# Kernel optimization log

Measured on AMD Instinct MI355X. Metric: run time of the kernel, lower is better.

The kernel has to match this reference:

```python
import jax, jax.numpy as jnp
import numpy as np

B, C, H, W = 16, 256, 64, 64
E = 8           # num_experts
TOPK = 2
HID = int(C * 2.0)  # hidden_mult = 2.0 -> 512


def setup_inputs() -> dict:
    key = jax.random.key(0)
    ks = jax.random.split(key, 6)
    x = jax.random.normal(ks[0], (B, C, H, W), dtype=jnp.float32)
    Wr = jax.random.normal(ks[1], (C, E), dtype=jnp.float32) * 0.02
    br = jnp.zeros((E,), dtype=jnp.float32)
    W1 = jax.random.normal(ks[2], (E, C, HID), dtype=jnp.float32) * 0.02
    b1 = jnp.zeros((E, HID), dtype=jnp.float32)
    W2 = jax.random.normal(ks[3], (E, HID, C), dtype=jnp.float32) * 0.02
    b2 = jnp.zeros((E, C), dtype=jnp.float32)
    # nn.Parameter(torch.zeros(1)) in the original; use a small random value so
    scale = jax.random.normal(ks[4], (1,), dtype=jnp.float32) * 0.1
    return {"x": x, "Wr": Wr, "br": br, "W1": W1, "b1": b1,
            "W2": W2, "b2": b2, "scale": scale}


def reference(x, Wr, br, W1, b1, W2, b2, scale):
    b, c, h, w = x.shape
    tokens = jnp.transpose(x, (0, 2, 3, 1)).reshape(b, h * w, c)  # (B, T, C)
    logits = tokens @ Wr + br                                      # (B, T, E)
    topv, topi = jax.lax.top_k(logits, TOPK)                       # (B, T, K)
    wts = jax.nn.softmax(topv, axis=-1)                            # (B, T, K)

    out = jnp.zeros_like(tokens)
    num_experts = Wr.shape[1]
    for e in range(num_experts):
        # combine weight for expert e: sum of routing weights where selected
        we = jnp.sum(jnp.where(topi == e, wts, 0.0), axis=-1)      # (B, T)
        hdn = jax.nn.gelu(tokens @ W1[e] + b1[e], approximate=False)
        y = hdn @ W2[e] + b2[e]                                    # (B, T, C)
        out = out + y * we[..., None]

    out = jnp.transpose(out.reshape(b, h, w, c), (0, 3, 1, 2))     # (B, C, H, W)
    return x + scale[0] * out
```

## Files before the change

### kernel.cpp

```cpp
#include <hip/hip_runtime.h>
#include <hip/hip_bf16.h>
#include <math.h>

#define HW   4096
#define CCH  256
#define NE   8
#define HID  512
#define NTOK 65536
#define PADH 260

typedef short s16x8 __attribute__((ext_vector_type(8)));
typedef float f32x4 __attribute__((ext_vector_type(4)));
typedef unsigned short u16x8 __attribute__((ext_vector_type(8)));

__device__ __forceinline__ float fast_gelu(float v) {
    float v2 = v * v;
    float s  = v * fmaf(0.10294324f, v2, 2.3022079f);
    float e  = exp2f(-s);
    return v * __builtin_amdgcn_rcpf(1.0f + e);
}

__device__ __forceinline__ float bfbits2f(unsigned short h) {
    return __uint_as_float(((unsigned)h) << 16);
}

__device__ __forceinline__ short f2bf_bits(float f) {
    __hip_bfloat16 b = __float2bfloat16(f);
    return *reinterpret_cast<short*>(&b);
}

__global__ __launch_bounds__(256) void k_transpose_both(
    const float* __restrict__ W1, const float* __restrict__ W2,
    __hip_bfloat16* __restrict__ w1t, __hip_bfloat16* __restrict__ w2t,
    int* __restrict__ meta)
{
    __shared__ float t[64][65];
    if (blockIdx.x == 0 && threadIdx.x < 16) meta[threadIdx.x] = 0;
    int bb = blockIdx.x;
    const float* in; __hip_bfloat16* out; int R, CC;
    if (bb < 256) { in = W1; out = w1t; R = 256; CC = 512; }
    else          { in = W2; out = w2t; R = 512; CC = 256; bb -= 256; }
    int tilesC = CC >> 6;
    int per = (R >> 6) * tilesC;
    int e = bb / per, tt = bb % per;
    int r0 = (tt / tilesC) << 6, c0 = (tt % tilesC) << 6;
    const float* ip = in + (size_t)e * R * CC;
    __hip_bfloat16* op = out + (size_t)e * R * CC;
    int lane = threadIdx.x & 63, g = threadIdx.x >> 6;
    for (int i = 0; i < 16; i++) {
        int r = i * 4 + g;
        t[r][lane] = ip[(size_t)(r0 + r) * CC + c0 + lane];
    }
    __syncthreads();
    for (int i = 0; i < 16; i++) {
        int r = i * 4 + g;
        op[(size_t)(c0 + r) * R + r0 + lane] = __float2bfloat16(t[lane][r]);
    }
}

__global__ __launch_bounds__(256) void k_router(
    const float* __restrict__ x, const float* __restrict__ Wr, const float* __restrict__ br,
    __hip_bfloat16* __restrict__ tokens, int* __restrict__ pair, float2* __restrict__ wts,
    int* __restrict__ meta )
{
    __shared__ float xt[CCH][66];
    __shared__ float wr[CCH][NE];
    __shared__ float lg[64][NE];
    __shared__ int lc[NE];
    int tid = threadIdx.x;
    int n0 = blockIdx.x * 64;
    int b = n0 >> 12, p0 = n0 & 4095;
    const float* xb = x + (size_t)b * CCH * HW + p0;
    for (int i = tid; i < CCH * NE; i += 256) ((float*)wr)[i] = Wr[i];
    if (tid < NE) lc[tid] = 0;
    int lane = tid & 63, wv = tid >> 6;
    {
        int j2 = tid & 31, cg = tid >> 5;
        for (int i = 0; i < 32; i++) {
            int c = cg + 8 * i;
            float2 v = *(const float2*)(xb + (size_t)c * HW + 2 * j2);
            *(float2*)&xt[c][2 * j2] = v;
        }
    }
    __syncthreads();
    float a0 = br[2 * wv], a1 = br[2 * wv + 1];
    for (int c = 0; c < CCH; c++) {
        float xv = xt[c][lane];
        a0 = fmaf(xv, wr[c][2 * wv], a0);
        a1 = fmaf(xv, wr[c][2 * wv + 1], a1);
    }
    lg[lane][2 * wv] = a0;
    lg[lane][2 * wv + 1] = a1;
    __syncthreads();
    if (wv == 0) {
        float v0 = -1e30f, v1 = -1e30f; int i0 = 0, i1 = 0;
        for (int e = 0; e < NE; e++) {
            float l = lg[lane][e];
            if (l > v0)      { v1 = v0; i1 = i0; v0 = l; i0 = e; }
            else if (l > v1) { v1 = l; i1 = e; }
        }
        float e1 = expf(v1 - v0);
        float s = 1.0f + e1;
        wts[n0 + lane] = make_float2(1.0f / s, e1 / s);
        pair[n0 + lane] = i0 | (i1 << 8);
        atomicAdd(&lc[i0], 1);
        atomicAdd(&lc[i1], 1);
    }
    __syncthreads();
    if (tid < NE && lc[tid] > 0) atomicAdd(&meta[tid], lc[tid]);
    {
        int r = tid & 63, gb = tid >> 6;
        for (int i = 0; i < 8; i++) {
            int c0 = gb * 64 + i * 8;
            s16x8 v;
#pragma unroll
            for (int j = 0; j < 8; j++) v[j] = f2bf_bits(xt[c0 + j][r]);
            *(s16x8*)(tokens + (size_t)(n0 + r) * CCH + c0) = v;
        }
    }
}

__global__ __launch_bounds__(256) void k_scatter(
    const int* __restrict__ pair, const float2* __restrict__ wts,
    int* __restrict__ meta, int* __restrict__ assign_tok, float* __restrict__ assign_w,
    int2* __restrict__ tok_slots)
{
    __shared__ int lcount[NE];
    __shared__ int lbase[NE];
    __shared__ int soff[NE];
    int tid = threadIdx.x;
    int n = blockIdx.x * 256 + tid;
    if (tid < NE) lcount[tid] = 0;
    __syncthreads();
    int pr = pair[n];
    int e0 = pr & 0xff, e1 = (pr >> 8) & 0xff;
    int p0 = atomicAdd(&lcount[e0], 1);
    int p1 = atomicAdd(&lcount[e1], 1);
    __syncthreads();
    if (tid == 0) {
        int off = 0, toff = 0;
        for (int ee = 0; ee < NE; ee++) {
            soff[ee] = off;
            int c = meta[ee];
            if (blockIdx.x == 0) { meta[16 + ee] = off; meta[25 + ee] = toff; }
            off += c;
            toff += (c + 63) >> 6;
        }
        if (blockIdx.x == 0) { meta[24] = off; meta[33] = toff; meta[34] = toff; }
    }
    if (tid < NE) lbase[tid] = atomicAdd(&meta[8 + tid], lcount[tid]);
    __syncthreads();
    float2 w = wts[n];
    int s0 = soff[e0] + lbase[e0] + p0;
    int s1 = soff[e1] + lbase[e1] + p1;
    assign_tok[s0] = n; assign_w[s0] = w.x;
    assign_tok[s1] = n; assign_w[s1] = w.y;
    tok_slots[n] = make_int2(s0, s1);
}

__global__ __launch_bounds__(512, 4) void k_expert(
    const __hip_bfloat16* __restrict__ tokens,
    const __hip_bfloat16* __restrict__ w1t,
    const __hip_bfloat16* __restrict__ w2t,
    const float* __restrict__ b1, const float* __restrict__ b2,
    const int* __restrict__ meta,
    const int* __restrict__ assign_tok, const float* __restrict__ assign_w,
    __hip_bfloat16* __restrict__ ybuf)
{
    __shared__ __align__(16) __hip_bfloat16 Af[64 * 256];
    __shared__ __align__(16) __hip_bfloat16 Hs[64 * PADH];
    __shared__ float wrow[64];
    __shared__ int trow[64];

    int total = meta[34];
    int swz = (int)blockIdx.x;
    int bid = (swz & 7) * 257 + (swz >> 3);
    if (bid >= total) return;
    int e = 0;
    while (e < 7 && bid >= meta[25 + e + 1]) e++;
    int tile = bid - meta[25 + e];
    int cnt = meta[e];
    int r0 = tile << 6;
    int abase = meta[16 + e] + r0;
    int nrows = cnt - r0; if (nrows > 64) nrows = 64;

    int tid = threadIdx.x;
    if (tid < 64) {
        if (tid < nrows) { trow[tid] = assign_tok[abase + tid]; wrow[tid] = assign_w[abase + tid]; }
        else             { trow[tid] = 0; wrow[tid] = 0.0f; }
    }
    __syncthreads();

    {
        uint4* dst = (uint4*)Af;
#pragma unroll
        for (int j = 0; j < 4; j++) {
            int row = j * 16 + (tid & 15);
            int chunk = (tid >> 4) & 31;
            dst[j * 512 + tid] = ((const uint4*)(tokens + (size_t)trow[row] * CCH))[chunk];
        }
    }

    int lane = tid & 63, wv = tid >> 6;
    int quad = lane >> 4, l15 = lane & 15;

    const __hip_bfloat16* w1e = w1t + (size_t)e * HID * CCH;
    const __hip_bfloat16* w2e = w2t + (size_t)e * CCH * HID;
    const float* b1e = b1 + e * HID;
    const float* b2e = b2 + e * CCH;

    const s16x8* apb = (const s16x8*)Af + quad * 16 + l15;

    auto G1Q = [&](int h, int off) {
        return (const s16x8*)(w1e + (size_t)(h * 256 + wv * 32 + off + l15) * CCH) + quad;
    };
    auto G2Q = [&](int h, int off) {
        return (const s16x8*)(w2e + (size_t)(wv * 32 + off + l15) * HID + h * 256) + quad;
    };

    int hfirst = (swz >> 8) & 1;

    f32x4 oacc[4][2];
#pragma unroll
    for (int i = 0; i < 4; i++)
#pragma unroll
        for (int j = 0; j < 2; j++) oacc[i][j] = (f32x4){0.f, 0.f, 0.f, 0.f};

    s16x8 bf0 = G1Q(hfirst, 0)[0], bf1 = G1Q(hfirst, 16)[0];
    float ob0 = b2e[wv * 32 + l15];
    float ob1 = b2e[wv * 32 + 16 + l15];

    __syncthreads();

#pragma unroll
    for (int hh = 0; hh < 2; hh++) {
        int h = hh ^ hfirst;
        const s16x8* bq0 = G1Q(h, 0);
        const s16x8* bq1 = G1Q(h, 16);

        f32x4 hacc[4][2];
#pragma unroll
        for (int i = 0; i < 4; i++)
#pragma unroll
            for (int j = 0; j < 2; j++) hacc[i][j] = (f32x4){0.f, 0.f, 0.f, 0.f};

#pragma unroll
        for (int kk = 0; kk < 8; kk++) {
            s16x8 bn0, bn1;
            if (kk < 7) { bn0 = bq0[(kk + 1) * 4]; bn1 = bq1[(kk + 1) * 4]; }
            s16x8 af[4];
#pragma unroll
            for (int mt = 0; mt < 4; mt++) af[mt] = apb[mt * 512 + kk * 4 * 16];
            __builtin_amdgcn_s_setprio(1);
#pragma unroll
            for (int mt = 0; mt < 4; mt++) {
                hacc[mt][0] = __builtin_amdgcn_mfma_f32_16x16x32_bf16(af[mt], bf0, hacc[mt][0], 0, 0, 0);
                hacc[mt][1] = __builtin_amdgcn_mfma_f32_16x16x32_bf16(af[mt], bf1, hacc[mt][1], 0, 0, 0);
            }
            __builtin_amdgcn_s_setprio(0);
            bf0 = bn0; bf1 = bn1;
        }

        const s16x8* b2q0 = G2Q(h, 0);
        const s16x8* b2q1 = G2Q(h, 16);
        s16x8 cf0 = b2q0[0], cf1 = b2q1[0];
        float biasA = b1e[h * 256 + wv * 32 + l15];
        float biasB = b1e[h * 256 + wv * 32 + 16 + l15];
        if (hh == 0) { int h2 = h ^ 1; bf0 = G1Q(h2, 0)[0]; bf1 = G1Q(h2, 16)[0]; }

        if (hh == 1) __syncthreads();

#pragma unroll
        for (int nt = 0; nt < 2; nt++) {
            int cl = wv * 32 + nt * 16 + l15;
            float bias = nt ? biasB : biasA;
#pragma unroll
            for (int mt = 0; mt < 4; mt++)
#pragma unroll
                for (int r = 0; r < 4; r++) {
                    int row = mt * 16 + quad * 4 + r;
                    float v = hacc[mt][nt][r] + bias;
                    Hs[row * PADH + cl] = __float2bfloat16(fast_gelu(v));
                }
        }
        __syncthreads();

#pragma unroll
        for (int kk = 0; kk < 8; kk++) {
            s16x8 cn0, cn1;
            if (kk < 7) { cn0 = b2q0[(kk + 1) * 4]; cn1 = b2q1[(kk + 1) * 4]; }
            s16x8 hf[4];
#pragma unroll
            for (int mt = 0; mt < 4; mt++)
                hf[mt] = *(const s16x8*)(Hs + (mt * 16 + l15) * PADH + kk * 32 + quad * 8);
            __builtin_amdgcn_s_setprio(1);
#pragma unroll
            for (int mt = 0; mt < 4; mt++) {
                oacc[mt][0] = __builtin_amdgcn_mfma_f32_16x16x32_bf16(hf[mt], cf0, oacc[mt][0], 0, 0, 0);
                oacc[mt][1] = __builtin_amdgcn_mfma_f32_16x16x32_bf16(hf[mt], cf1, oacc[mt][1], 0, 0, 0);
            }
            __builtin_amdgcn_s_setprio(0);
            cf0 = cn0; cf1 = cn1;
        }
    }

#pragma unroll
    for (int nt = 0; nt < 2; nt++) {
        int cc = wv * 32 + nt * 16 + l15;
        float bias = nt ? ob1 : ob0;
#pragma unroll
        for (int mt = 0; mt < 4; mt++) {
#pragma unroll
            for (int r = 0; r < 4; r++) {
                int row = mt * 16 + quad * 4 + r;
                if (row < nrows) {
                    float v = (oacc[mt][nt][r] + bias) * wrow[row];
                    ybuf[(size_t)(abase + row) * CCH + cc] = __float2bfloat16(v);
                }
            }
        }
    }
}

__global__ __launch_bounds__(256) void k_combine(
    const float* __restrict__ x, const __hip_bfloat16* __restrict__ ybuf,
    const int2* __restrict__ tok_slots, const float* __restrict__ scale,
    float* __restrict__ out)
{
    __shared__ float moe[CCH][33];
    __shared__ int2 slots[32];
    int tid = threadIdx.x;
    int n0 = blockIdx.x * 32;
    if (tid < 32) slots[tid] = tok_slots[n0 + tid];
    __syncthreads();
    {
        int r = tid & 31, g0 = tid >> 5;
#pragma unroll
        for (int it = 0; it < 2; it++) {
            int g = g0 + 8 * it;
            int2 s = slots[r];
            const u16x8* px = (const u16x8*)(ybuf + (size_t)s.x * CCH + 16 * g);
            const u16x8* py = (const u16x8*)(ybuf + (size_t)s.y * CCH + 16 * g);
            u16x8 ax0 = px[0], ax1 = px[1], ay0 = py[0], ay1 = py[1];
#pragma unroll
            for (int k = 0; k < 8; k++) {
                moe[16 * g + k][r]     = bfbits2f(ax0[k]) + bfbits2f(ay0[k]);
                moe[16 * g + 8 + k][r] = bfbits2f(ax1[k]) + bfbits2f(ay1[k]);
            }
        }
    }
    __syncthreads();
    float sc = scale[0];
    int b = n0 >> 12, p0 = n0 & 4095;
    const float* xb = x + (size_t)b * CCH * HW + p0;
    float* ob = out + (size_t)b * CCH * HW + p0;
    int j = tid & 7, cbase = tid >> 3;
#pragma unroll
    for (int i = 0; i < 8; i++) {
        int c = cbase + 32 * i;
        float4 xv = *(const float4*)(xb + (size_t)c * HW + 4 * j);
        float4 o;
        o.x = xv.x + sc * moe[c][4 * j];
        o.y = xv.y + sc * moe[c][4 * j + 1];
        o.z = xv.z + sc * moe[c][4 * j + 2];
        o.w = xv.w + sc * moe[c][4 * j + 3];
        *(float4*)(ob + (size_t)c * HW + 4 * j) = o;
    }
}

extern "C" void kernel_launch(void* const* d_in, const int* in_sizes, int n_in,
                              void* d_out, int out_size, void* d_ws, size_t ws_size,
                              hipStream_t stream)
{
    const float* x     = (const float*)d_in[0];
    const float* Wr    = (const float*)d_in[1];
    const float* br    = (const float*)d_in[2];
    const float* W1    = (const float*)d_in[3];
    const float* b1    = (const float*)d_in[4];
    const float* W2    = (const float*)d_in[5];
    const float* b2    = (const float*)d_in[6];
    const float* scale = (const float*)d_in[7];
    float* out = (float*)d_out;

    char* ws = (char*)d_ws;
    __hip_bfloat16* tokens = (__hip_bfloat16*)(ws);
    __hip_bfloat16* w1t    = (__hip_bfloat16*)(ws + 33554432);
    __hip_bfloat16* w2t    = (__hip_bfloat16*)(ws + 35651584);
    __hip_bfloat16* ybuf   = (__hip_bfloat16*)(ws + 37748736);
    int*    assign_tok = (int*)   (ws + 104857600);
    float*  assign_w   = (float*) (ws + 105381888);
    int2*   tok_slots  = (int2*)  (ws + 105906176);
    int*    pair       = (int*)   (ws + 106430464);
    float2* wts        = (float2*)(ws + 106692608);
    int*    meta       = (int*)   (ws + 107216896);

    k_transpose_both<<<512, 256, 0, stream>>>(W1, W2, w1t, w2t, meta);
    k_router<<<1024, 256, 0, stream>>>(x, Wr, br, tokens, pair, wts, meta);
    k_scatter<<<256, 256, 0, stream>>>(pair, wts, meta, assign_tok, assign_w, tok_slots);
    k_expert<<<2056, 512, 0, stream>>>(tokens, w1t, w2t, b1, b2, meta,
                                       assign_tok, assign_w, ybuf);
    k_combine<<<2048, 256, 0, stream>>>(x, ybuf, tok_slots, scale, out);
}
```

Baseline: 343.5 us.

## Restructure router into 32-token blocks, store combine staging as bf16, drop h swizzle

```diff
diff --git a/kernel.cpp b/kernel.cpp
--- a/kernel.cpp
+++ b/kernel.cpp
@@ -12,6 +12,7 @@
 typedef short s16x8 __attribute__((ext_vector_type(8)));
 typedef float f32x4 __attribute__((ext_vector_type(4)));
 typedef unsigned short u16x8 __attribute__((ext_vector_type(8)));
+typedef unsigned short u16x4 __attribute__((ext_vector_type(4)));
 
 __device__ __forceinline__ float fast_gelu(float v) {
     float v2 = v * v;
@@ -27,6 +28,11 @@
 __device__ __forceinline__ short f2bf_bits(float f) {
     __hip_bfloat16 b = __float2bfloat16(f);
     return *reinterpret_cast<short*>(&b);
+}
+
+__device__ __forceinline__ unsigned short f2bf_ubits(float f) {
+    __hip_bfloat16 b = __float2bfloat16(f);
+    return *reinterpret_cast<unsigned short*>(&b);
 }
 
 __global__ __launch_bounds__(256) void k_transpose_both(
@@ -63,60 +69,72 @@
     __hip_bfloat16* __restrict__ tokens, int* __restrict__ pair, float2* __restrict__ wts,
     int* __restrict__ meta )
 {
-    __shared__ float xt[CCH][66];
-    __shared__ float wr[CCH][NE];
-    __shared__ float lg[64][NE];
+    __shared__ float xt[CCH][33];
+    __shared__ float wrp[2304];
+    __shared__ float lg[32][NE];
     __shared__ int lc[NE];
     int tid = threadIdx.x;
-    int n0 = blockIdx.x * 64;
+    int n0 = blockIdx.x * 32;
     int b = n0 >> 12, p0 = n0 & 4095;
     const float* xb = x + (size_t)b * CCH * HW + p0;
-    for (int i = tid; i < CCH * NE; i += 256) ((float*)wr)[i] = Wr[i];
+    for (int i = tid; i < CCH * NE; i += 256) wrp[i] = Wr[i];
     if (tid < NE) lc[tid] = 0;
-    int lane = tid & 63, wv = tid >> 6;
+    __syncthreads();
+    int j = tid & 31, cg = tid >> 5;
+    float pacc[8];
+#pragma unroll
+    for (int e = 0; e < 8; e++) pacc[e] = 0.f;
+    for (int i = 0; i < 32; i++) {
+        int c = cg + 8 * i;
+        float xv = xb[(size_t)c * HW + j];
+        xt[c][j] = xv;
+        const float4* wp = (const float4*)(wrp + c * 8);
+        float4 wa = wp[0], wb2 = wp[1];
+        pacc[0] = fmaf(xv, wa.x, pacc[0]);
+        pacc[1] = fmaf(xv, wa.y, pacc[1]);
+        pacc[2] = fmaf(xv, wa.z, pacc[2]);
+        pacc[3] = fmaf(xv, wa.w, pacc[3]);
+        pacc[4] = fmaf(xv, wb2.x, pacc[4]);
+        pacc[5] = fmaf(xv, wb2.y, pacc[5]);
+        pacc[6] = fmaf(xv, wb2.z, pacc[6]);
+        pacc[7] = fmaf(xv, wb2.w, pacc[7]);
+    }
+    __syncthreads();
+    float* plg = wrp;
+#pragma unroll
+    for (int e = 0; e < 8; e++) plg[(cg * 32 + j) * 9 + e] = pacc[e];
+    __syncthreads();
     {
-        int j2 = tid & 31, cg = tid >> 5;
-        for (int i = 0; i < 32; i++) {
-            int c = cg + 8 * i;
-            float2 v = *(const float2*)(xb + (size_t)c * HW + 2 * j2);
-            *(float2*)&xt[c][2 * j2] = v;
-        }
-    }
-    __syncthreads();
-    float a0 = br[2 * wv], a1 = br[2 * wv + 1];
-    for (int c = 0; c < CCH; c++) {
-        float xv = xt[c][lane];
-        a0 = fmaf(xv, wr[c][2 * wv], a0);
-        a1 = fmaf(xv, wr[c][2 * wv + 1], a1);
-    }
-    lg[lane][2 * wv] = a0;
-    lg[lane][2 * wv + 1] = a1;
-    __syncthreads();
-    if (wv == 0) {
+        int jj = tid & 31, e = tid >> 5;
+        float s = br[e];
+#pragma unroll
+        for (int g = 0; g < 8; g++) s += plg[(g * 32 + jj) * 9 + e];
+        lg[jj][e] = s;
+    }
+    __syncthreads();
+    if (tid < 32) {
         float v0 = -1e30f, v1 = -1e30f; int i0 = 0, i1 = 0;
         for (int e = 0; e < NE; e++) {
-            float l = lg[lane][e];
+            float l = lg[tid][e];
             if (l > v0)      { v1 = v0; i1 = i0; v0 = l; i0 = e; }
             else if (l > v1) { v1 = l; i1 = e; }
         }
         float e1 = expf(v1 - v0);
         float s = 1.0f + e1;
-        wts[n0 + lane] = make_float2(1.0f / s, e1 / s);
-        pair[n0 + lane] = i0 | (i1 << 8);
+        wts[n0 + tid] = make_float2(1.0f / s, e1 / s);
+        pair[n0 + tid] = i0 | (i1 << 8);
         atomicAdd(&lc[i0], 1);
         atomicAdd(&lc[i1], 1);
     }
     __syncthreads();
     if (tid < NE && lc[tid] > 0) atomicAdd(&meta[tid], lc[tid]);
-    {
-        int r = tid & 63, gb = tid >> 6;
-        for (int i = 0; i < 8; i++) {
-            int c0 = gb * 64 + i * 8;
-            s16x8 v;
-#pragma unroll
-            for (int j = 0; j < 8; j++) v[j] = f2bf_bits(xt[c0 + j][r]);
-            *(s16x8*)(tokens + (size_t)(n0 + r) * CCH + c0) = v;
-        }
+#pragma unroll
+    for (int i = 0; i < 4; i++) {
+        int c0 = (cg + 8 * i) * 8;
+        s16x8 v;
+#pragma unroll
+        for (int k = 0; k < 8; k++) v[k] = f2bf_bits(xt[c0 + k][j]);
+        *(s16x8*)(tokens + (size_t)(n0 + j) * CCH + c0) = v;
     }
 }
 
@@ -218,23 +236,20 @@
         return (const s16x8*)(w2e + (size_t)(wv * 32 + off + l15) * HID + h * 256) + quad;
     };
 
-    int hfirst = (swz >> 8) & 1;
-
     f32x4 oacc[4][2];
 #pragma unroll
     for (int i = 0; i < 4; i++)
 #pragma unroll
         for (int j = 0; j < 2; j++) oacc[i][j] = (f32x4){0.f, 0.f, 0.f, 0.f};
 
-    s16x8 bf0 = G1Q(hfirst, 0)[0], bf1 = G1Q(hfirst, 16)[0];
+    s16x8 bf0 = G1Q(0, 0)[0], bf1 = G1Q(0, 16)[0];
     float ob0 = b2e[wv * 32 + l15];
     float ob1 = b2e[wv * 32 + 16 + l15];
 
     __syncthreads();
 
 #pragma unroll
-    for (int hh = 0; hh < 2; hh++) {
-        int h = hh ^ hfirst;
+    for (int h = 0; h < 2; h++) {
         const s16x8* bq0 = G1Q(h, 0);
         const s16x8* bq1 = G1Q(h, 16);
 
@@ -266,9 +281,9 @@
         s16x8 cf0 = b2q0[0], cf1 = b2q1[0];
         float biasA = b1e[h * 256 + wv * 32 + l15];
         float biasB = b1e[h * 256 + wv * 32 + 16 + l15];
-        if (hh == 0) { int h2 = h ^ 1; bf0 = G1Q(h2, 0)[0]; bf1 = G1Q(h2, 16)[0]; }
-
-        if (hh == 1) __syncthreads();
+        if (h == 0) { bf0 = G1Q(1, 0)[0]; bf1 = G1Q(1, 16)[0]; }
+
+        if (h == 1) __syncthreads();
 
 #pragma unroll
         for (int nt = 0; nt < 2; nt++) {
@@ -327,7 +342,7 @@
     const int2* __restrict__ tok_slots, const float* __restrict__ scale,
     float* __restrict__ out)
 {
-    __shared__ float moe[CCH][33];
+    __shared__ __align__(16) unsigned short moe[CCH][36];
     __shared__ int2 slots[32];
     int tid = threadIdx.x;
     int n0 = blockIdx.x * 32;
@@ -344,8 +359,8 @@
             u16x8 ax0 = px[0], ax1 = px[1], ay0 = py[0], ay1 = py[1];
 #pragma unroll
             for (int k = 0; k < 8; k++) {
-                moe[16 * g + k][r]     = bfbits2f(ax0[k]) + bfbits2f(ay0[k]);
-                moe[16 * g + 8 + k][r] = bfbits2f(ax1[k]) + bfbits2f(ay1[k]);
+                moe[16 * g + k][r]     = f2bf_ubits(bfbits2f(ax0[k]) + bfbits2f(ay0[k]));
+                moe[16 * g + 8 + k][r] = f2bf_ubits(bfbits2f(ax1[k]) + bfbits2f(ay1[k]));
             }
         }
     }
@@ -359,11 +374,12 @@
     for (int i = 0; i < 8; i++) {
         int c = cbase + 32 * i;
         float4 xv = *(const float4*)(xb + (size_t)c * HW + 4 * j);
+        u16x4 mv = *(const u16x4*)&moe[c][4 * j];
         float4 o;
-        o.x = xv.x + sc * moe[c][4 * j];
-        o.y = xv.y + sc * moe[c][4 * j + 1];
-        o.z = xv.z + sc * moe[c][4 * j + 2];
-        o.w = xv.w + sc * moe[c][4 * j + 3];
+        o.x = xv.x + sc * bfbits2f(mv[0]);
+        o.y = xv.y + sc * bfbits2f(mv[1]);
+        o.z = xv.z + sc * bfbits2f(mv[2]);
+        o.w = xv.w + sc * bfbits2f(mv[3]);
         *(float4*)(ob + (size_t)c * HW + 4 * j) = o;
     }
 }
@@ -395,7 +411,7 @@
     int*    meta       = (int*)   (ws + 107216896);
 
     k_transpose_both<<<512, 256, 0, stream>>>(W1, W2, w1t, w2t, meta);
-    k_router<<<1024, 256, 0, stream>>>(x, Wr, br, tokens, pair, wts, meta);
+    k_router<<<2048, 256, 0, stream>>>(x, Wr, br, tokens, pair, wts, meta);
     k_scatter<<<256, 256, 0, stream>>>(pair, wts, meta, assign_tok, assign_w, tok_slots);
     k_expert<<<2056, 512, 0, stream>>>(tokens, w1t, w2t, b1, b2, meta,
                                        assign_tok, assign_w, ybuf);
```

Result: no change. 340.6 us (-0.9%).
